# Performance work log

Hardware: AMD Instinct MI355X
Metric: run time of the kernel (lower is better)

Reference implementation:

```python
import jax, jax.numpy as jnp
import numpy as np

E = 1024
FF = 4096
B, S = 4, 2048
EPS = 1e-5

def _layernorm(x, g, b):
    m = jnp.mean(x, axis=-1, keepdims=True)
    v = jnp.var(x, axis=-1, keepdims=True)
    return (x - m) * jax.lax.rsqrt(v + EPS) * g + b

def setup_inputs() -> dict:
    key = jax.random.key(0)
    ks = jax.random.split(key, 16)
    def lin(k, fan_in, shape):
        bound = 1.0 / np.sqrt(fan_in)
        return jax.random.uniform(k, shape, jnp.float32, -bound, bound)
    return {
        "src_embs": jax.random.normal(ks[0], (B, S, E), jnp.float32),
        "Wq_w": lin(ks[1], E, (E, E)), "Wq_b": lin(ks[2], E, (E,)),
        "Wk_w": lin(ks[3], E, (E, E)), "Wk_b": lin(ks[4], E, (E,)),
        "Wv_w": lin(ks[5], E, (E, E)), "Wv_b": lin(ks[6], E, (E,)),
        "Wo_w": lin(ks[7], E, (E, E)), "Wo_b": lin(ks[8], E, (E,)),
        "W1_w": lin(ks[9], E, (FF, E)), "W1_b": lin(ks[10], E, (FF,)),
        "W2_w": lin(ks[11], FF, (E, FF)), "W2_b": lin(ks[12], FF, (E,)),
        "g1": jnp.ones((E,), jnp.float32), "b1": jnp.zeros((E,), jnp.float32),
        "g2": jnp.ones((E,), jnp.float32), "b2": jnp.zeros((E,), jnp.float32),
        "g3": jnp.ones((E,), jnp.float32), "b3": jnp.zeros((E,), jnp.float32),
    }

def reference(src_embs, Wq_w, Wq_b, Wk_w, Wk_b, Wv_w, Wv_b, Wo_w, Wo_b,
              W1_w, W1_b, W2_w, W2_b, g1, b1, g2, b2, g3, b3):
    x = _layernorm(src_embs, g1, b1)
    Q = x @ Wq_w.T + Wq_b
    K = x @ Wk_w.T + Wk_b
    V = x @ Wv_w.T + Wv_b
    # single-head attention, scaled by sqrt(embed_dim) per source
    scores = jnp.einsum('bqe,bke->bqk', Q, K) / jnp.sqrt(jnp.float32(E))
    attn = jax.nn.softmax(scores, axis=-1)
    attn_out = jnp.einsum('bqk,bke->bqe', attn, V) @ Wo_w.T + Wo_b
    h = src_embs + attn_out
    hn = _layernorm(h, g2, b2)
    ff = jax.nn.relu(hn @ W1_w.T + W1_b) @ W2_w.T + W2_b
    out = h + ff
    return _layernorm(out, g3, b3)
```

## Files before the change

### kernel.cpp

```cpp
#include <hip/hip_runtime.h>
#include <cstdint>
#include <cmath>

#define E_DIM 1024
#define FF_DIM 4096
#define B_DIM 4
#define S_DIM 2048
#define NTOK (B_DIM * S_DIM)
#define QKV_N 3072

typedef __bf16 bf16;
typedef __attribute__((ext_vector_type(8))) __bf16 bf16x8;
typedef __attribute__((ext_vector_type(4))) float f32x4;

__device__ __forceinline__ void gload_lds16(const void* g, void* l) {
  __builtin_amdgcn_global_load_lds(
      (const __attribute__((address_space(1))) unsigned int*)g,
      (__attribute__((address_space(3))) unsigned int*)l, 16, 0, 0);
}

__device__ __forceinline__ float waveRedSum(float v) {
#pragma unroll
  for (int o = 32; o > 0; o >>= 1) v += __shfl_xor(v, o, 64);
  return v;
}
__device__ __forceinline__ float waveRedMax(float v) {
#pragma unroll
  for (int o = 32; o > 0; o >>= 1) v = fmaxf(v, __shfl_xor(v, o, 64));
  return v;
}

__global__ __launch_bounds__(256) void cvt_k(const float* __restrict__ in,
                                             bf16* __restrict__ out, int n4) {
  int i = blockIdx.x * 256 + threadIdx.x;
  if (i < n4) {
    float4 v = reinterpret_cast<const float4*>(in)[i];
    bf16* o = out + (size_t)i * 4;
    o[0] = (bf16)v.x; o[1] = (bf16)v.y; o[2] = (bf16)v.z; o[3] = (bf16)v.w;
  }
}

template <typename OutT>
__global__ __launch_bounds__(256) void layernorm_k(const float* __restrict__ x,
                                                   OutT* __restrict__ out,
                                                   const float* __restrict__ g,
                                                   const float* __restrict__ b) {
  const int row = blockIdx.x;
  const int tid = threadIdx.x;
  const float4 v = reinterpret_cast<const float4*>(x + (size_t)row * E_DIM)[tid];
  float s = v.x + v.y + v.z + v.w;
  float q = v.x * v.x + v.y * v.y + v.z * v.z + v.w * v.w;
  s = waveRedSum(s);
  q = waveRedSum(q);
  __shared__ float sa[4], sb[4];
  const int lane = tid & 63, wid = tid >> 6;
  if (lane == 0) { sa[wid] = s; sb[wid] = q; }
  __syncthreads();
  s = sa[0] + sa[1] + sa[2] + sa[3];
  q = sb[0] + sb[1] + sb[2] + sb[3];
  const float mean = s * (1.0f / E_DIM);
  const float var = q * (1.0f / E_DIM) - mean * mean;
  const float rstd = rsqrtf(var + 1e-5f);
  const int c = tid * 4;
  OutT* op = out + (size_t)row * E_DIM + c;
  const float vv[4] = {v.x, v.y, v.z, v.w};
#pragma unroll
  for (int j = 0; j < 4; ++j)
    op[j] = (OutT)((vv[j] - mean) * rstd * g[c + j] + b[c + j]);
}

__global__ __launch_bounds__(256) void ln2_fused_k(
    const float* __restrict__ src, const bf16* __restrict__ p0,
    const bf16* __restrict__ p1, const float* __restrict__ bo,
    float* __restrict__ h, bf16* __restrict__ hn,
    const float* __restrict__ g, const float* __restrict__ b) {
  const int row = blockIdx.x;
  const int tid = threadIdx.x;
  const int c = tid * 4;
  const float4 sv = reinterpret_cast<const float4*>(src + (size_t)row * E_DIM)[tid];
  const ushort4 a0 = reinterpret_cast<const ushort4*>(p0 + (size_t)row * E_DIM)[tid];
  const ushort4 a1 = reinterpret_cast<const ushort4*>(p1 + (size_t)row * E_DIM)[tid];
  const float4 bv = reinterpret_cast<const float4*>(bo)[tid];
  auto b2f = [](unsigned short u) {
    union { unsigned int i; float f; } t; t.i = (unsigned int)u << 16; return t.f;
  };
  float x[4];
  x[0] = sv.x + b2f(a0.x) + b2f(a1.x) + bv.x;
  x[1] = sv.y + b2f(a0.y) + b2f(a1.y) + bv.y;
  x[2] = sv.z + b2f(a0.z) + b2f(a1.z) + bv.z;
  x[3] = sv.w + b2f(a0.w) + b2f(a1.w) + bv.w;
  float4 hv = {x[0], x[1], x[2], x[3]};
  reinterpret_cast<float4*>(h + (size_t)row * E_DIM)[tid] = hv;
  float s = x[0] + x[1] + x[2] + x[3];
  float q = x[0] * x[0] + x[1] * x[1] + x[2] * x[2] + x[3] * x[3];
  s = waveRedSum(s);
  q = waveRedSum(q);
  __shared__ float sa[4], sb[4];
  const int lane = tid & 63, wid = tid >> 6;
  if (lane == 0) { sa[wid] = s; sb[wid] = q; }
  __syncthreads();
  s = sa[0] + sa[1] + sa[2] + sa[3];
  q = sb[0] + sb[1] + sb[2] + sb[3];
  const float mean = s * (1.0f / E_DIM);
  const float var = q * (1.0f / E_DIM) - mean * mean;
  const float rstd = rsqrtf(var + 1e-5f);
  bf16* op = hn + (size_t)row * E_DIM + c;
#pragma unroll
  for (int j = 0; j < 4; ++j)
    op[j] = (bf16)((x[j] - mean) * rstd * g[c + j] + b[c + j]);
}

__global__ __launch_bounds__(256) void ln3_fused_k(
    const float* __restrict__ h, const bf16* __restrict__ p0,
    const bf16* __restrict__ p1, const float* __restrict__ bias2,
    float* __restrict__ out, const float* __restrict__ g,
    const float* __restrict__ b) {
  const int row = blockIdx.x;
  const int tid = threadIdx.x;
  const int c = tid * 4;
  const float4 hv = reinterpret_cast<const float4*>(h + (size_t)row * E_DIM)[tid];
  const ushort4 a0 = reinterpret_cast<const ushort4*>(p0 + (size_t)row * E_DIM)[tid];
  const ushort4 a1 = reinterpret_cast<const ushort4*>(p1 + (size_t)row * E_DIM)[tid];
  const float4 bv = reinterpret_cast<const float4*>(bias2)[tid];
  auto b2f = [](unsigned short u) {
    union { unsigned int i; float f; } t; t.i = (unsigned int)u << 16; return t.f;
  };
  float x[4];
  x[0] = hv.x + b2f(a0.x) + b2f(a1.x) + bv.x;
  x[1] = hv.y + b2f(a0.y) + b2f(a1.y) + bv.y;
  x[2] = hv.z + b2f(a0.z) + b2f(a1.z) + bv.z;
  x[3] = hv.w + b2f(a0.w) + b2f(a1.w) + bv.w;
  float s = x[0] + x[1] + x[2] + x[3];
  float q = x[0] * x[0] + x[1] * x[1] + x[2] * x[2] + x[3] * x[3];
  s = waveRedSum(s);
  q = waveRedSum(q);
  __shared__ float sa[4], sb[4];
  const int lane = tid & 63, wid = tid >> 6;
  if (lane == 0) { sa[wid] = s; sb[wid] = q; }
  __syncthreads();
  s = sa[0] + sa[1] + sa[2] + sa[3];
  q = sb[0] + sb[1] + sb[2] + sb[3];
  const float mean = s * (1.0f / E_DIM);
  const float var = q * (1.0f / E_DIM) - mean * mean;
  const float rstd = rsqrtf(var + 1e-5f);
  float* op = out + (size_t)row * E_DIM + c;
#pragma unroll
  for (int j = 0; j < 4; ++j)
    op[j] = (x[j] - mean) * rstd * g[c + j] + b[c + j];
}

__global__ __launch_bounds__(256) void softmax_k(bf16* __restrict__ scores) {
  const int row = blockIdx.x;
  bf16* rp = scores + (size_t)row * S_DIM;
  const int tid = threadIdx.x;
  const int lane = tid & 63, wid = tid >> 6;
  bf16x8 v8 = *reinterpret_cast<const bf16x8*>(rp + tid * 8);
  float v[8];
#pragma unroll
  for (int j = 0; j < 8; ++j) v[j] = (float)v8[j];
  float mx = v[0];
#pragma unroll
  for (int j = 1; j < 8; ++j) mx = fmaxf(mx, v[j]);
  mx = waveRedMax(mx);
  __shared__ float sm_[4], ss_[4];
  if (lane == 0) sm_[wid] = mx;
  __syncthreads();
  mx = fmaxf(fmaxf(sm_[0], sm_[1]), fmaxf(sm_[2], sm_[3]));
  float e[8];
  float s = 0.f;
#pragma unroll
  for (int j = 0; j < 8; ++j) { e[j] = __expf(v[j] - mx); s += e[j]; }
  s = waveRedSum(s);
  if (lane == 0) ss_[wid] = s;
  __syncthreads();
  s = ss_[0] + ss_[1] + ss_[2] + ss_[3];
  const float inv = 1.0f / s;
  bf16x8 o;
#pragma unroll
  for (int j = 0; j < 8; ++j) o[j] = (bf16)(e[j] * inv);
  *reinterpret_cast<bf16x8*>(rp + tid * 8) = o;
}

__global__ __launch_bounds__(256) void transpose_k(const bf16* __restrict__ in,
                                                   int ld_in, size_t bstride_in,
                                                   bf16* __restrict__ out) {
  __shared__ bf16 t[32][33];
  const int b = blockIdx.z;
  const bf16* ip = in + (size_t)b * bstride_in;
  bf16* op = out + (size_t)b * S_DIM * E_DIM;
  const int e0 = blockIdx.x * 32, s0 = blockIdx.y * 32;
  const int tx = threadIdx.x & 31, ty = threadIdx.x >> 5;
#pragma unroll
  for (int r = 0; r < 32; r += 8)
    t[ty + r][tx] = ip[(size_t)(s0 + ty + r) * ld_in + e0 + tx];
  __syncthreads();
#pragma unroll
  for (int r = 0; r < 32; r += 8)
    op[(size_t)(e0 + ty + r) * S_DIM + s0 + tx] = t[tx][ty + r];
}

template <int BN, typename OutT, bool RELU>
__global__ __launch_bounds__(512) void gemm8p_k(
    const bf16* __restrict__ A0, int lda, const bf16* __restrict__ Bt0, int ldb,
    OutT* __restrict__ C0, int ldc, int M, int N, int K,
    const float* __restrict__ bias, const float* __restrict__ resid, int ldr,
    float scale, size_t sAz, size_t sBz, size_t sCz) {
  constexpr int BM = 256;
  constexpr int NCH_B = BN / 64;
  constexpr int NCH = 4 + NCH_B;
  constexpr int DEPTH = (BN == 256) ? 2 : 3;
  constexpr int DBUF = (BM + BN) * 128;
  __shared__ __align__(16) char smem[DEPTH * DBUF];

  const int tid = threadIdx.x;
  const int lane = tid & 63;
  const int wid = tid >> 6;

  const bf16* A = A0 + (size_t)blockIdx.z * sAz;
  const bf16* Bt = Bt0 + (size_t)blockIdx.z * sBz;
  OutT* C = C0 + (size_t)blockIdx.z * sCz;

  const int gx = gridDim.x;
  const int nwg = gx * gridDim.y;
  int wg = blockIdx.y * gx + blockIdx.x;
  {
    const int q = nwg >> 3, r8 = nwg & 7;
    const int xcd = wg & 7, lin = wg >> 3;
    wg = (xcd < r8 ? xcd * (q + 1) : r8 * (q + 1) + (xcd - r8) * q) + lin;
  }
  const int m0 = (wg / gx) * 256;
  const int n0 = (wg % gx) * BN;

  auto stage_chunk = [&](int t, int c) {
    char* base = smem + (t % DEPTH) * DBUF;
    const int r8 = tid >> 3;
    const int gg = tid & 7;
    if (c < NCH_B) {
      const int row = c * 64 + r8;
      const int g = gg ^ (row & 7);
      gload_lds16(Bt + (size_t)(n0 + row) * ldb + t * 64 + g * 8,
                  base + BM * 128 + c * 8192 + wid * 1024);
    } else {
      const int i = c - NCH_B;
      const int ca = ((i & 1) << 1) | (i >> 1);
      const int row = ca * 64 + r8;
      const int g = gg ^ (row & 7);
      gload_lds16(A + (size_t)(m0 + row) * lda + t * 64 + g * 8,
                  base + ca * 8192 + wid * 1024);
    }
  };

  f32x4 accQ[2][4][2][2] = {};
  f32x4 accH[4][4] = {};

  const int NT = K >> 6;
  if constexpr (BN == 256) {
#pragma unroll
    for (int c = 0; c < NCH; ++c) stage_chunk(0, c);
    asm volatile("s_waitcnt vmcnt(2)" ::: "memory");
  } else {
#pragma unroll
    for (int c = 0; c < NCH; ++c) stage_chunk(0, c);
#pragma unroll
    for (int c = 0; c < NCH; ++c) stage_chunk(1, c);
    asm volatile("s_waitcnt vmcnt(6)" ::: "memory");
  }
  __builtin_amdgcn_s_barrier();

  for (int t = 0; t < NT; ++t) {
    const char* lA = smem + (t % DEPTH) * DBUF;
    const char* lB = lA + BM * 128;
    if constexpr (BN == 256) {
      const int wr = wid >> 2;
      const int wc = wid & 3;
      bf16x8 af[4][2];
      bf16x8 bfv[2][2][2];
#pragma unroll
      for (int p = 0; p < 4; ++p) {
        const int mh = p >> 1, nh = p & 1;
        if (p == 0 || p == 2) {
#pragma unroll
          for (int fm = 0; fm < 4; ++fm) {
            const int row = wr * 128 + mh * 64 + fm * 16 + (lane & 15);
#pragma unroll
            for (int ks = 0; ks < 2; ++ks) {
              const int g = ((ks << 2) | (lane >> 4)) ^ (row & 7);
              af[fm][ks] = *reinterpret_cast<const bf16x8*>(lA + row * 128 + g * 16);
            }
          }
        }
        if (p < 2) {
#pragma unroll
          for (int fn = 0; fn < 2; ++fn) {
            const int row = wc * 64 + p * 32 + fn * 16 + (lane & 15);
#pragma unroll
            for (int ks = 0; ks < 2; ++ks) {
              const int g = ((ks << 2) | (lane >> 4)) ^ (row & 7);
              bfv[p][fn][ks] =
                  *reinterpret_cast<const bf16x8*>(lB + row * 128 + g * 16);
            }
          }
        }
        if (t + 1 < NT) {
#pragma unroll
          for (int c = 0; c < 2; ++c) stage_chunk(t + 1, p * 2 + c);
        }
        __builtin_amdgcn_s_barrier();
        __builtin_amdgcn_s_setprio(1);
#pragma unroll
        for (int fm = 0; fm < 4; ++fm)
#pragma unroll
          for (int fn = 0; fn < 2; ++fn) {
            accQ[mh][fm][nh][fn] = __builtin_amdgcn_mfma_f32_16x16x32_bf16(
                af[fm][0], bfv[nh][fn][0], accQ[mh][fm][nh][fn], 0, 0, 0);
            accQ[mh][fm][nh][fn] = __builtin_amdgcn_mfma_f32_16x16x32_bf16(
                af[fm][1], bfv[nh][fn][1], accQ[mh][fm][nh][fn], 0, 0, 0);
          }
        __builtin_amdgcn_s_setprio(0);
        if (p == 1) {
          if (t + 1 < NT) asm volatile("s_waitcnt vmcnt(4)" ::: "memory");
          else            asm volatile("s_waitcnt vmcnt(0)" ::: "memory");
        }
        if (p == 3) {
          asm volatile("s_waitcnt vmcnt(2)" ::: "memory");
        }
        __builtin_amdgcn_s_barrier();
      }
    } else {
      const int wr = wid >> 1;
      const int wc = wid & 1;
#pragma unroll
      for (int p = 0; p < 2; ++p) {
        bf16x8 af[4], bf[4];
#pragma unroll
        for (int fm = 0; fm < 4; ++fm) {
          const int row = wr * 64 + fm * 16 + (lane & 15);
          const int g = ((p << 2) | (lane >> 4)) ^ (row & 7);
          af[fm] = *reinterpret_cast<const bf16x8*>(lA + row * 128 + g * 16);
        }
#pragma unroll
        for (int fn = 0; fn < 4; ++fn) {
          const int row = wc * 64 + fn * 16 + (lane & 15);
          const int g = ((p << 2) | (lane >> 4)) ^ (row & 7);
          bf[fn] = *reinterpret_cast<const bf16x8*>(lB + row * 128 + g * 16);
        }
        if (t + 2 < NT) {
#pragma unroll
          for (int c = 0; c < 3; ++c) stage_chunk(t + 2, p * 3 + c);
        }
        __builtin_amdgcn_s_barrier();
        __builtin_amdgcn_s_setprio(1);
#pragma unroll
        for (int fm = 0; fm < 4; ++fm)
#pragma unroll
          for (int fn = 0; fn < 4; ++fn)
            accH[fm][fn] = __builtin_amdgcn_mfma_f32_16x16x32_bf16(
                af[fm], bf[fn], accH[fm][fn], 0, 0, 0);
        __builtin_amdgcn_s_setprio(0);
        if (p == 1) {
          if (t + 2 < NT) asm volatile("s_waitcnt vmcnt(6)" ::: "memory");
          else            asm volatile("s_waitcnt vmcnt(0)" ::: "memory");
        }
        __builtin_amdgcn_s_barrier();
      }
    }
  }

  if constexpr (BN == 256) {
    const int wr = wid >> 2, wc = wid & 3;
#pragma unroll
    for (int mh = 0; mh < 2; ++mh)
#pragma unroll
      for (int nh = 0; nh < 2; ++nh)
#pragma unroll
        for (int fn = 0; fn < 2; ++fn) {
          const int col = n0 + wc * 64 + nh * 32 + fn * 16 + (lane & 15);
          const float bv = bias ? bias[col] : 0.0f;
#pragma unroll
          for (int fm = 0; fm < 4; ++fm)
#pragma unroll
            for (int i = 0; i < 4; ++i) {
              const int row = m0 + wr * 128 + mh * 64 + fm * 16 + (lane >> 4) * 4 + i;
              float v = accQ[mh][fm][nh][fn][i] * scale + bv;
              if (resid) v += resid[(size_t)row * ldr + col];
              if (RELU) v = fmaxf(v, 0.0f);
              C[(size_t)row * ldc + col] = (OutT)v;
            }
        }
  } else {
    const int wr = wid >> 1, wc = wid & 1;
#pragma unroll
    for (int fn = 0; fn < 4; ++fn) {
      const int col = n0 + wc * 64 + fn * 16 + (lane & 15);
      const float bv = bias ? bias[col] : 0.0f;
#pragma unroll
      for (int fm = 0; fm < 4; ++fm)
#pragma unroll
        for (int i = 0; i < 4; ++i) {
          const int row = m0 + wr * 64 + fm * 16 + (lane >> 4) * 4 + i;
          float v = accH[fm][fn][i] * scale + bv;
          if (resid) v += resid[(size_t)row * ldr + col];
          if (RELU) v = fmaxf(v, 0.0f);
          C[(size_t)row * ldc + col] = (OutT)v;
        }
    }
  }
}

extern "C" void kernel_launch(void* const* d_in, const int* in_sizes, int n_in,
                              void* d_out, int out_size, void* d_ws,
                              size_t ws_size, hipStream_t stream) {
  const float* src = (const float*)d_in[0];
  const float* Wq_w = (const float*)d_in[1];
  const float* Wq_b = (const float*)d_in[2];
  const float* Wk_w = (const float*)d_in[3];
  const float* Wk_b = (const float*)d_in[4];
  const float* Wv_w = (const float*)d_in[5];
  const float* Wv_b = (const float*)d_in[6];
  const float* Wo_w = (const float*)d_in[7];
  const float* Wo_b = (const float*)d_in[8];
  const float* W1_w = (const float*)d_in[9];
  const float* W1_b = (const float*)d_in[10];
  const float* W2_w = (const float*)d_in[11];
  const float* W2_b = (const float*)d_in[12];
  const float* g1 = (const float*)d_in[13];
  const float* b1 = (const float*)d_in[14];
  const float* g2 = (const float*)d_in[15];
  const float* b2 = (const float*)d_in[16];
  const float* g3 = (const float*)d_in[17];
  const float* b3 = (const float*)d_in[18];
  float* out = (float*)d_out;
  (void)ws_size; (void)in_sizes; (void)n_in; (void)out_size;

  const size_t MB = 1ull << 20;
  char* ws = (char*)d_ws;
  bf16* wqkv = (bf16*)(ws + 0 * MB);
  bf16* wo = (bf16*)(ws + 6 * MB);
  bf16* w1 = (bf16*)(ws + 8 * MB);
  bf16* w2 = (bf16*)(ws + 16 * MB);
  bf16* Cqkv = (bf16*)(ws + 24 * MB);
  bf16* Vt = (bf16*)(ws + 72 * MB);
  bf16* scoresB = (bf16*)(ws + 88 * MB);
  bf16* xln = (bf16*)(ws + 88 * MB);
  float* bqkv = (float*)(ws + 104 * MB);
  bf16* ctx = Cqkv;
  bf16* pw = (bf16*)(ws + 40 * MB);
  bf16* hn = scoresB;
  bf16* f1 = (bf16*)(ws + 24 * MB);
  bf16* pp = (bf16*)(ws + 88 * MB);
  float* h = out;

  cvt_k<<<(E_DIM * E_DIM / 4 + 255) / 256, 256, 0, stream>>>(Wq_w, wqkv, E_DIM * E_DIM / 4);
  cvt_k<<<(E_DIM * E_DIM / 4 + 255) / 256, 256, 0, stream>>>(Wk_w, wqkv + (size_t)E_DIM * E_DIM, E_DIM * E_DIM / 4);
  cvt_k<<<(E_DIM * E_DIM / 4 + 255) / 256, 256, 0, stream>>>(Wv_w, wqkv + 2 * (size_t)E_DIM * E_DIM, E_DIM * E_DIM / 4);
  cvt_k<<<(E_DIM * E_DIM / 4 + 255) / 256, 256, 0, stream>>>(Wo_w, wo, E_DIM * E_DIM / 4);
  cvt_k<<<(FF_DIM * E_DIM / 4 + 255) / 256, 256, 0, stream>>>(W1_w, w1, FF_DIM * E_DIM / 4);
  cvt_k<<<(FF_DIM * E_DIM / 4 + 255) / 256, 256, 0, stream>>>(W2_w, w2, FF_DIM * E_DIM / 4);
  hipMemcpyAsync(bqkv, Wq_b, E_DIM * 4, hipMemcpyDeviceToDevice, stream);
  hipMemcpyAsync(bqkv + E_DIM, Wk_b, E_DIM * 4, hipMemcpyDeviceToDevice, stream);
  hipMemcpyAsync(bqkv + 2 * E_DIM, Wv_b, E_DIM * 4, hipMemcpyDeviceToDevice, stream);

  layernorm_k<bf16><<<NTOK, 256, 0, stream>>>(src, xln, g1, b1);

  dim3 gQKV(QKV_N / 256, NTOK / 256);
  gemm8p_k<256, bf16, false><<<gQKV, 512, 0, stream>>>(
      xln, E_DIM, wqkv, E_DIM, Cqkv, QKV_N, NTOK, QKV_N, E_DIM,
      bqkv, nullptr, 0, 1.0f, 0, 0, 0);

  dim3 gSc(S_DIM / 256, S_DIM / 256, B_DIM);
  gemm8p_k<256, bf16, false><<<gSc, 512, 0, stream>>>(
      Cqkv, QKV_N, Cqkv + E_DIM, QKV_N, scoresB, S_DIM, S_DIM, S_DIM, E_DIM,
      nullptr, nullptr, 0, 1.0f / 32.0f,
      (size_t)S_DIM * QKV_N, (size_t)S_DIM * QKV_N, (size_t)S_DIM * S_DIM);

  softmax_k<<<B_DIM * S_DIM, 256, 0, stream>>>(scoresB);

  transpose_k<<<dim3(E_DIM / 32, S_DIM / 32, B_DIM), 256, 0, stream>>>(
      Cqkv + 2 * E_DIM, QKV_N, (size_t)S_DIM * QKV_N, Vt);

  dim3 gPV(E_DIM / 128, S_DIM / 256, B_DIM);
  gemm8p_k<128, bf16, false><<<gPV, 512, 0, stream>>>(
      scoresB, S_DIM, Vt, S_DIM, ctx, E_DIM, S_DIM, E_DIM, S_DIM,
      nullptr, nullptr, 0, 1.0f,
      (size_t)S_DIM * S_DIM, (size_t)S_DIM * E_DIM, (size_t)S_DIM * E_DIM);

  dim3 gWo(E_DIM / 256, NTOK / 256, 2);
  gemm8p_k<256, bf16, false><<<gWo, 512, 0, stream>>>(
      ctx, E_DIM, wo, E_DIM, pw, E_DIM, NTOK, E_DIM, E_DIM / 2,
      nullptr, nullptr, 0, 1.0f,
      (size_t)(E_DIM / 2), (size_t)(E_DIM / 2), (size_t)NTOK * E_DIM);

  ln2_fused_k<<<NTOK, 256, 0, stream>>>(
      src, pw, pw + (size_t)NTOK * E_DIM, Wo_b, h, hn, g2, b2);

  dim3 gF1(FF_DIM / 256, NTOK / 256);
  gemm8p_k<256, bf16, true><<<gF1, 512, 0, stream>>>(
      hn, E_DIM, w1, E_DIM, f1, FF_DIM, NTOK, FF_DIM, E_DIM,
      W1_b, nullptr, 0, 1.0f, 0, 0, 0);

  dim3 gF2(E_DIM / 256, NTOK / 256, 2);
  gemm8p_k<256, bf16, false><<<gF2, 512, 0, stream>>>(
      f1, FF_DIM, w2, FF_DIM, pp, E_DIM, NTOK, E_DIM, FF_DIM / 2,
      nullptr, nullptr, 0, 1.0f,
      (size_t)(FF_DIM / 2), (size_t)(FF_DIM / 2), (size_t)NTOK * E_DIM);

  ln3_fused_k<<<NTOK, 256, 0, stream>>>(
      h, pp, pp + (size_t)NTOK * E_DIM, W2_b, out, g3, b3);
}
```

Before: 396.3 us.

## Stage BN=256 GEMM tiles through registers instead of direct global-to-LDS loads

For the 256x256 GEMM tile path, the global_load_lds direct-to-LDS staging is replaced by ordinary global loads into registers, which are later written to LDS. The four sub-phases of each K step are unrolled by hand, and global prefetches and LDS writes for the next tile are interleaved between MFMA phases. The aim is finer control over load/compute overlap and waitcnt placement. The cost is extra VGPR pressure, added LDS write instructions and more barriers per K step.

```diff
diff --git a/kernel.cpp b/kernel.cpp
--- a/kernel.cpp
+++ b/kernel.cpp
@@ -206,8 +206,6 @@
     const float* __restrict__ bias, const float* __restrict__ resid, int ldr,
     float scale, size_t sAz, size_t sBz, size_t sCz) {
   constexpr int BM = 256;
-  constexpr int NCH_B = BN / 64;
-  constexpr int NCH = 4 + NCH_B;
   constexpr int DEPTH = (BN == 256) ? 2 : 3;
   constexpr int DBUF = (BM + BN) * 128;
   __shared__ __align__(16) char smem[DEPTH * DBUF];
@@ -224,109 +222,234 @@
   const int nwg = gx * gridDim.y;
   int wg = blockIdx.y * gx + blockIdx.x;
   {
-    const int q = nwg >> 3, r8 = nwg & 7;
+    const int q = nwg >> 3, r8_ = nwg & 7;
     const int xcd = wg & 7, lin = wg >> 3;
-    wg = (xcd < r8 ? xcd * (q + 1) : r8 * (q + 1) + (xcd - r8) * q) + lin;
+    wg = (xcd < r8_ ? xcd * (q + 1) : r8_ * (q + 1) + (xcd - r8_) * q) + lin;
   }
   const int m0 = (wg / gx) * 256;
   const int n0 = (wg % gx) * BN;
 
-  auto stage_chunk = [&](int t, int c) {
-    char* base = smem + (t % DEPTH) * DBUF;
-    const int r8 = tid >> 3;
-    const int gg = tid & 7;
-    if (c < NCH_B) {
-      const int row = c * 64 + r8;
-      const int g = gg ^ (row & 7);
-      gload_lds16(Bt + (size_t)(n0 + row) * ldb + t * 64 + g * 8,
-                  base + BM * 128 + c * 8192 + wid * 1024);
-    } else {
-      const int i = c - NCH_B;
-      const int ca = ((i & 1) << 1) | (i >> 1);
-      const int row = ca * 64 + r8;
-      const int g = gg ^ (row & 7);
-      gload_lds16(A + (size_t)(m0 + row) * lda + t * 64 + g * 8,
-                  base + ca * 8192 + wid * 1024);
-    }
-  };
-
   f32x4 accQ[2][4][2][2] = {};
   f32x4 accH[4][4] = {};
 
   const int NT = K >> 6;
+
   if constexpr (BN == 256) {
-#pragma unroll
-    for (int c = 0; c < NCH; ++c) stage_chunk(0, c);
-    asm volatile("s_waitcnt vmcnt(2)" ::: "memory");
+    const int wr = wid >> 2;
+    const int wc = wid & 3;
+    const int r8 = tid >> 3, gg = tid & 7;
+    const int gsw = gg ^ (r8 & 7);
+    const bf16* pB0 = Bt + (size_t)(n0 + r8) * ldb + gsw * 8;
+    const bf16* pA0 = A + (size_t)(m0 + r8) * lda + gsw * 8;
+    const size_t ldb64 = (size_t)64 * ldb, lda64 = (size_t)64 * lda;
+    const int lw = tid * 16;
+
+    int4 ge0, ge1, go0, go1;
+
+    ge0 = *reinterpret_cast<const int4*>(pB0);
+    ge1 = *reinterpret_cast<const int4*>(pB0 + ldb64);
+    go0 = *reinterpret_cast<const int4*>(pB0 + 2 * ldb64);
+    go1 = *reinterpret_cast<const int4*>(pB0 + 3 * ldb64);
+    *reinterpret_cast<int4*>(smem + BM * 128 + 0 * 8192 + lw) = ge0;
+    *reinterpret_cast<int4*>(smem + BM * 128 + 1 * 8192 + lw) = ge1;
+    ge0 = *reinterpret_cast<const int4*>(pA0);
+    ge1 = *reinterpret_cast<const int4*>(pA0 + 2 * lda64);
+    *reinterpret_cast<int4*>(smem + BM * 128 + 2 * 8192 + lw) = go0;
+    *reinterpret_cast<int4*>(smem + BM * 128 + 3 * 8192 + lw) = go1;
+    go0 = *reinterpret_cast<const int4*>(pA0 + 1 * lda64);
+    go1 = *reinterpret_cast<const int4*>(pA0 + 3 * lda64);
+    *reinterpret_cast<int4*>(smem + 0 * 8192 + lw) = ge0;
+    *reinterpret_cast<int4*>(smem + 2 * 8192 + lw) = ge1;
+    *reinterpret_cast<int4*>(smem + 1 * 8192 + lw) = go0;
+    *reinterpret_cast<int4*>(smem + 3 * 8192 + lw) = go1;
+    asm volatile("s_waitcnt lgkmcnt(0)" ::: "memory");
+    __builtin_amdgcn_s_barrier();
+
+    for (int t = 0; t < NT; ++t) {
+      char* cur = smem + (t & 1) * DBUF;
+      char* nxt = smem + ((t + 1) & 1) * DBUF;
+      const char* lB = cur + BM * 128;
+      const bool pf = (t + 1 < NT);
+      const int tk = (t + 1) * 64;
+      bf16x8 af[4][2], bf[2][2];
+      if (pf) {
+        ge0 = *reinterpret_cast<const int4*>(pB0 + tk);
+        ge1 = *reinterpret_cast<const int4*>(pB0 + ldb64 + tk);
+        __builtin_amdgcn_sched_barrier(0);
+      }
+#pragma unroll
+      for (int fm = 0; fm < 4; ++fm) {
+        const int row = wr * 128 + 0 * 64 + fm * 16 + (lane & 15);
+#pragma unroll
+        for (int ks = 0; ks < 2; ++ks) {
+          const int g = ((ks << 2) | (lane >> 4)) ^ (row & 7);
+          af[fm][ks] = *reinterpret_cast<const bf16x8*>(cur + row * 128 + g * 16);
+        }
+      }
+#pragma unroll
+      for (int fn = 0; fn < 2; ++fn) {
+        const int row = wc * 64 + 0 * 32 + fn * 16 + (lane & 15);
+#pragma unroll
+        for (int ks = 0; ks < 2; ++ks) {
+          const int g = ((ks << 2) | (lane >> 4)) ^ (row & 7);
+          bf[fn][ks] = *reinterpret_cast<const bf16x8*>(lB + row * 128 + g * 16);
+        }
+      }
+      __builtin_amdgcn_s_barrier();
+      __builtin_amdgcn_s_setprio(1);
+#pragma unroll
+      for (int fm = 0; fm < 4; ++fm)
+#pragma unroll
+        for (int fn = 0; fn < 2; ++fn) {
+          accQ[0][fm][0][fn] = __builtin_amdgcn_mfma_f32_16x16x32_bf16(
+              af[fm][0], bf[fn][0], accQ[0][fm][0][fn], 0, 0, 0);
+          accQ[0][fm][0][fn] = __builtin_amdgcn_mfma_f32_16x16x32_bf16(
+              af[fm][1], bf[fn][1], accQ[0][fm][0][fn], 0, 0, 0);
+        }
+      __builtin_amdgcn_s_setprio(0);
+      if (t > 0) {
+        *reinterpret_cast<int4*>(cur + 1 * 8192 + lw) = go0;
+        *reinterpret_cast<int4*>(cur + 3 * 8192 + lw) = go1;
+        asm volatile("s_waitcnt lgkmcnt(0)" ::: "memory");
+      }
+      __builtin_amdgcn_s_barrier();
+      if (pf) {
+        go0 = *reinterpret_cast<const int4*>(pB0 + 2 * ldb64 + tk);
+        go1 = *reinterpret_cast<const int4*>(pB0 + 3 * ldb64 + tk);
+        __builtin_amdgcn_sched_barrier(0);
+      }
+#pragma unroll
+      for (int fn = 0; fn < 2; ++fn) {
+        const int row = wc * 64 + 1 * 32 + fn * 16 + (lane & 15);
+#pragma unroll
+        for (int ks = 0; ks < 2; ++ks) {
+          const int g = ((ks << 2) | (lane >> 4)) ^ (row & 7);
+          bf[fn][ks] = *reinterpret_cast<const bf16x8*>(lB + row * 128 + g * 16);
+        }
+      }
+      __builtin_amdgcn_s_barrier();
+      __builtin_amdgcn_s_setprio(1);
+#pragma unroll
+      for (int fm = 0; fm < 4; ++fm)
+#pragma unroll
+        for (int fn = 0; fn < 2; ++fn) {
+          accQ[0][fm][1][fn] = __builtin_amdgcn_mfma_f32_16x16x32_bf16(
+              af[fm][0], bf[fn][0], accQ[0][fm][1][fn], 0, 0, 0);
+          accQ[0][fm][1][fn] = __builtin_amdgcn_mfma_f32_16x16x32_bf16(
+              af[fm][1], bf[fn][1], accQ[0][fm][1][fn], 0, 0, 0);
+        }
+      __builtin_amdgcn_s_setprio(0);
+      if (pf) {
+        *reinterpret_cast<int4*>(nxt + BM * 128 + 0 * 8192 + lw) = ge0;
+        *reinterpret_cast<int4*>(nxt + BM * 128 + 1 * 8192 + lw) = ge1;
+        asm volatile("s_waitcnt lgkmcnt(0)" ::: "memory");
+      }
+      __builtin_amdgcn_s_barrier();
+      if (pf) {
+        ge0 = *reinterpret_cast<const int4*>(pA0 + tk);
+        ge1 = *reinterpret_cast<const int4*>(pA0 + 2 * lda64 + tk);
+        __builtin_amdgcn_sched_barrier(0);
+      }
+#pragma unroll
+      for (int fm = 0; fm < 4; ++fm) {
+        const int row = wr * 128 + 1 * 64 + fm * 16 + (lane & 15);
+#pragma unroll
+        for (int ks = 0; ks < 2; ++ks) {
+          const int g = ((ks << 2) | (lane >> 4)) ^ (row & 7);
+          af[fm][ks] = *reinterpret_cast<const bf16x8*>(cur + row * 128 + g * 16);
+        }
+      }
+#pragma unroll
+      for (int fn = 0; fn < 2; ++fn) {
+        const int row = wc * 64 + 0 * 32 + fn * 16 + (lane & 15);
+#pragma unroll
+        for (int ks = 0; ks < 2; ++ks) {
+          const int g = ((ks << 2) | (lane >> 4)) ^ (row & 7);
+          bf[fn][ks] = *reinterpret_cast<const bf16x8*>(lB + row * 128 + g * 16);
+        }
+      }
+      __builtin_amdgcn_s_barrier();
+      __builtin_amdgcn_s_setprio(1);
+#pragma unroll
+      for (int fm = 0; fm < 4; ++fm)
+#pragma unroll
+        for (int fn = 0; fn < 2; ++fn) {
+          accQ[1][fm][0][fn] = __builtin_amdgcn_mfma_f32_16x16x32_bf16(
+              af[fm][0], bf[fn][0], accQ[1][fm][0][fn], 0, 0, 0);
+          accQ[1][fm][0][fn] = __builtin_amdgcn_mfma_f32_16x16x32_bf16(
+              af[fm][1], bf[fn][1], accQ[1][fm][0][fn], 0, 0, 0);
+        }
+      __builtin_amdgcn_s_setprio(0);
+      if (pf) {
+        *reinterpret_cast<int4*>(nxt + BM * 128 + 2 * 8192 + lw) = go0;
+        *reinterpret_cast<int4*>(nxt + BM * 128 + 3 * 8192 + lw) = go1;
+        asm volatile("s_waitcnt lgkmcnt(0)" ::: "memory");
+      }
+      __builtin_amdgcn_s_barrier();
+      if (pf) {
+        go0 = *reinterpret_cast<const int4*>(pA0 + 1 * lda64 + tk);
+        go1 = *reinterpret_cast<const int4*>(pA0 + 3 * lda64 + tk);
+        __builtin_amdgcn_sched_barrier(0);
+      }
+#pragma unroll
+      for (int fn = 0; fn < 2; ++fn) {
+        const int row = wc * 64 + 1 * 32 + fn * 16 + (lane & 15);
+#pragma unroll
+        for (int ks = 0; ks < 2; ++ks) {
+          const int g = ((ks << 2) | (lane >> 4)) ^ (row & 7);
+          bf[fn][ks] = *reinterpret_cast<const bf16x8*>(lB + row * 128 + g * 16);
+        }
+      }
+      __builtin_amdgcn_s_barrier();
+      __builtin_amdgcn_s_setprio(1);
+#pragma unroll
+      for (int fm = 0; fm < 4; ++fm)
+#pragma unroll
+        for (int fn = 0; fn < 2; ++fn) {
+          accQ[1][fm][1][fn] = __builtin_amdgcn_mfma_f32_16x16x32_bf16(
+              af[fm][0], bf[fn][0], accQ[1][fm][1][fn], 0, 0, 0);
+          accQ[1][fm][1][fn] = __builtin_amdgcn_mfma_f32_16x16x32_bf16(
+              af[fm][1], bf[fn][1], accQ[1][fm][1][fn], 0, 0, 0);
+        }
+      __builtin_amdgcn_s_setprio(0);
+      if (pf) {
+        *reinterpret_cast<int4*>(nxt + 0 * 8192 + lw) = ge0;
+        *reinterpret_cast<int4*>(nxt + 2 * 8192 + lw) = ge1;
+        asm volatile("s_waitcnt lgkmcnt(0)" ::: "memory");
+      }
+      __builtin_amdgcn_s_barrier();
+    }
   } else {
+    constexpr int NCH_B = BN / 64;
+    constexpr int NCH = 4 + NCH_B;
+    auto stage_chunk = [&](int t, int c) {
+      char* base = smem + (t % DEPTH) * DBUF;
+      const int r8 = tid >> 3;
+      const int gg = tid & 7;
+      if (c < NCH_B) {
+        const int row = c * 64 + r8;
+        const int g = gg ^ (row & 7);
+        gload_lds16(Bt + (size_t)(n0 + row) * ldb + t * 64 + g * 8,
+                    base + BM * 128 + c * 8192 + wid * 1024);
+      } else {
+        const int i = c - NCH_B;
+        const int ca = ((i & 1) << 1) | (i >> 1);
+        const int row = ca * 64 + r8;
+        const int g = gg ^ (row & 7);
+        gload_lds16(A + (size_t)(m0 + row) * lda + t * 64 + g * 8,
+                    base + ca * 8192 + wid * 1024);
+      }
+    };
 #pragma unroll
     for (int c = 0; c < NCH; ++c) stage_chunk(0, c);
 #pragma unroll
     for (int c = 0; c < NCH; ++c) stage_chunk(1, c);
     asm volatile("s_waitcnt vmcnt(6)" ::: "memory");
-  }
-  __builtin_amdgcn_s_barrier();
-
-  for (int t = 0; t < NT; ++t) {
-    const char* lA = smem + (t % DEPTH) * DBUF;
-    const char* lB = lA + BM * 128;
-    if constexpr (BN == 256) {
-      const int wr = wid >> 2;
-      const int wc = wid & 3;
-      bf16x8 af[4][2];
-      bf16x8 bfv[2][2][2];
-#pragma unroll
-      for (int p = 0; p < 4; ++p) {
-        const int mh = p >> 1, nh = p & 1;
-        if (p == 0 || p == 2) {
-#pragma unroll
-          for (int fm = 0; fm < 4; ++fm) {
-            const int row = wr * 128 + mh * 64 + fm * 16 + (lane & 15);
-#pragma unroll
-            for (int ks = 0; ks < 2; ++ks) {
-              const int g = ((ks << 2) | (lane >> 4)) ^ (row & 7);
-              af[fm][ks] = *reinterpret_cast<const bf16x8*>(lA + row * 128 + g * 16);
-            }
-          }
-        }
-        if (p < 2) {
-#pragma unroll
-          for (int fn = 0; fn < 2; ++fn) {
-            const int row = wc * 64 + p * 32 + fn * 16 + (lane & 15);
-#pragma unroll
-            for (int ks = 0; ks < 2; ++ks) {
-              const int g = ((ks << 2) | (lane >> 4)) ^ (row & 7);
-              bfv[p][fn][ks] =
-                  *reinterpret_cast<const bf16x8*>(lB + row * 128 + g * 16);
-            }
-          }
-        }
-        if (t + 1 < NT) {
-#pragma unroll
-          for (int c = 0; c < 2; ++c) stage_chunk(t + 1, p * 2 + c);
-        }
-        __builtin_amdgcn_s_barrier();
-        __builtin_amdgcn_s_setprio(1);
-#pragma unroll
-        for (int fm = 0; fm < 4; ++fm)
-#pragma unroll
-          for (int fn = 0; fn < 2; ++fn) {
-            accQ[mh][fm][nh][fn] = __builtin_amdgcn_mfma_f32_16x16x32_bf16(
-                af[fm][0], bfv[nh][fn][0], accQ[mh][fm][nh][fn], 0, 0, 0);
-            accQ[mh][fm][nh][fn] = __builtin_amdgcn_mfma_f32_16x16x32_bf16(
-                af[fm][1], bfv[nh][fn][1], accQ[mh][fm][nh][fn], 0, 0, 0);
-          }
-        __builtin_amdgcn_s_setprio(0);
-        if (p == 1) {
-          if (t + 1 < NT) asm volatile("s_waitcnt vmcnt(4)" ::: "memory");
-          else            asm volatile("s_waitcnt vmcnt(0)" ::: "memory");
-        }
-        if (p == 3) {
-          asm volatile("s_waitcnt vmcnt(2)" ::: "memory");
-        }
-        __builtin_amdgcn_s_barrier();
-      }
-    } else {
+    __builtin_amdgcn_s_barrier();
+
+    for (int t = 0; t < NT; ++t) {
+      const char* lA = smem + (t % DEPTH) * DBUF;
+      const char* lB = lA + BM * 128;
       const int wr = wid >> 1;
       const int wc = wid & 1;
 #pragma unroll
```

New measurement: 428.0 us. 8.0% more time.
